# Kernel optimization log

Measured on AMD Instinct MI355X. Metric: run time of the kernel, lower is better.

Reference implementation:

```python
import jax, jax.numpy as jnp
import numpy as np

B, N, D = 32, 2048, 1024


def setup_inputs() -> dict:
    key = jax.random.key(0)
    k1, k2, k3, k4, k5, k6 = jax.random.split(key, 6)
    encoded = jax.random.normal(k1, (B, N, D), dtype=jnp.float32)
    decoder_state = jax.random.normal(k2, (B, D), dtype=jnp.float32)
    mask = jax.random.randint(k3, (B, N), 0, 2, dtype=jnp.int32)
    scale = 1.0 / np.sqrt(D)
    W1 = jax.random.normal(k4, (D, D), dtype=jnp.float32) * scale  # applied as x @ W1
    W2 = jax.random.normal(k5, (D, D), dtype=jnp.float32) * scale
    vt = jax.random.normal(k6, (D,), dtype=jnp.float32) * scale
    return {"encoded": encoded, "decoder_state": decoder_state, "mask": mask,
            "W1": W1, "W2": W2, "vt": vt}


def reference(encoded, decoder_state, mask, W1, W2, vt):
    temperature = 1.0
    # process_encoded: W1(encoded)  [B, N, D]
    enc = jnp.einsum('bnd,de->bne', encoded, W1)
    # W2(decoder_state)  [B, D] -> broadcast-add over N
    dec = decoder_state @ W2
    # vt(tanh(.)).squeeze(2)  -> logits [B, N]
    u = jnp.einsum('bnd,d->bn', jnp.tanh(enc + dec[:, None, :]), vt)
    # masked log-softmax with temperature over dim=1
    logits = u / temperature + jnp.log(mask.astype(u.dtype) + 1e-45)
    return jax.nn.log_softmax(logits, axis=1)
```

## Files before the change

### kernel.cpp

```cpp
#include <hip/hip_runtime.h>

typedef _Float16 half8 __attribute__((ext_vector_type(8)));
typedef __fp16   pk2   __attribute__((ext_vector_type(2)));
typedef float    f32x4 __attribute__((ext_vector_type(4)));

#define GLOBAL_AS __attribute__((address_space(1)))
#define LDS_AS    __attribute__((address_space(3)))

static constexpr int Bb = 32;
static constexpr int Nn = 2048;
static constexpr int Dd = 1024;
static constexpr int M  = Bb * Nn;

__global__ void prep_w1(const float* __restrict__ W1, _Float16* __restrict__ W1TT) {
    int g = blockIdx.x * 256 + threadIdx.x;
    int tile = g >> 9;
    int u = g & 511;
    int et = tile >> 5, kt = tile & 31;
    int q = u >> 7, e = u & 127;
    int d0 = kt * 32 + q * 8;
    int col = et * 128 + e;
    half8 h;
#pragma unroll
    for (int j = 0; j < 8; ++j)
        h[j] = (_Float16)W1[(size_t)(d0 + j) * Dd + col];
    *(half8*)(W1TT + (size_t)g * 8) = h;
}

__global__ void dec_kernel(const float* __restrict__ ds, const float* __restrict__ W2,
                           float* __restrict__ dec) {
    __shared__ float part[4][64];
    int b = blockIdx.x, ech = blockIdx.y;
    int tid = threadIdx.x;
    int e = ech * 64 + (tid & 63);
    int dc = tid >> 6;
    float acc = 0.f;
#pragma unroll 4
    for (int d = dc * 256; d < dc * 256 + 256; ++d)
        acc += ds[b * Dd + d] * W2[(size_t)d * Dd + e];
    part[dc][tid & 63] = acc;
    __syncthreads();
    if (tid < 64)
        dec[b * Dd + e] = part[0][tid] + part[1][tid] + part[2][tid] + part[3][tid];
}

__global__ __launch_bounds__(256) void gemm_fused(
    const float* __restrict__ A,
    const _Float16* __restrict__ W1TT,
    const float* __restrict__ dec,
    const float* __restrict__ vt,
    float* __restrict__ u_part)
{
    __shared__ _Float16 As2[4 * 128 * 8];
    __shared__ _Float16 Bs2[512 * 8];
    __shared__ float usum[2][128];

    const int et = blockIdx.x;
    const int mtile = blockIdx.y;
    const int tid = threadIdx.x;
    const int lane = tid & 63, wid = tid >> 6;
    const int wm = wid & 1, we = wid >> 1;
    const int q = lane >> 4, l15 = lane & 15;

    f32x4 acc[4][4] = {};

    const int arow = tid >> 1, khalf = tid & 1;
    const float* aptr = A + (size_t)(mtile * 128 + arow) * Dd + khalf * 16;
    const int q0 = khalf * 2;
    const _Float16* bbase = W1TT + (size_t)et * 32 * 512 * 8
                            + ((size_t)(wid * 2) * 64 + lane) * 8;
    _Float16* bdst0 = &Bs2[(wid * 2 + 0) * 64 * 8];
    _Float16* bdst1 = &Bs2[(wid * 2 + 1) * 64 * 8];

#pragma unroll 1
    for (int kt = 0; kt < 32; ++kt) {
        const _Float16* bk = bbase + (size_t)kt * 512 * 8;
        __builtin_amdgcn_global_load_lds((const GLOBAL_AS void*)bk,
                                         (LDS_AS void*)bdst0, 16, 0, 0);
        __builtin_amdgcn_global_load_lds((const GLOBAL_AS void*)(bk + 64 * 8),
                                         (LDS_AS void*)bdst1, 16, 0, 0);
        const float4* ap = (const float4*)(aptr + kt * 32);
        float4 f0 = ap[0], f1 = ap[1], f2 = ap[2], f3 = ap[3];
        half8 h0, h1;
        {
            pk2 t;
            t = __builtin_amdgcn_cvt_pkrtz(f0.x, f0.y); h0[0] = t[0]; h0[1] = t[1];
            t = __builtin_amdgcn_cvt_pkrtz(f0.z, f0.w); h0[2] = t[0]; h0[3] = t[1];
            t = __builtin_amdgcn_cvt_pkrtz(f1.x, f1.y); h0[4] = t[0]; h0[5] = t[1];
            t = __builtin_amdgcn_cvt_pkrtz(f1.z, f1.w); h0[6] = t[0]; h0[7] = t[1];
            t = __builtin_amdgcn_cvt_pkrtz(f2.x, f2.y); h1[0] = t[0]; h1[1] = t[1];
            t = __builtin_amdgcn_cvt_pkrtz(f2.z, f2.w); h1[2] = t[0]; h1[3] = t[1];
            t = __builtin_amdgcn_cvt_pkrtz(f3.x, f3.y); h1[4] = t[0]; h1[5] = t[1];
            t = __builtin_amdgcn_cvt_pkrtz(f3.z, f3.w); h1[6] = t[0]; h1[7] = t[1];
        }
        *(half8*)&As2[((q0 + 0) * 128 + arow) * 8] = h0;
        *(half8*)&As2[((q0 + 1) * 128 + arow) * 8] = h1;
        __syncthreads();

        half8 af[4], bf[4];
#pragma unroll
        for (int mt = 0; mt < 4; ++mt)
            af[mt] = *(const half8*)&As2[(q * 128 + wm * 64 + mt * 16 + l15) * 8];
#pragma unroll
        for (int nt = 0; nt < 4; ++nt)
            bf[nt] = *(const half8*)&Bs2[(q * 128 + we * 64 + nt * 16 + l15) * 8];
#pragma unroll
        for (int mt = 0; mt < 4; ++mt)
#pragma unroll
            for (int nt = 0; nt < 4; ++nt)
                acc[mt][nt] = __builtin_amdgcn_mfma_f32_16x16x32_f16(
                    af[mt], bf[nt], acc[mt][nt], 0, 0, 0);
        __syncthreads();
    }

    const int b = mtile >> 4;
    float vtv[4], dcv[4];
#pragma unroll
    for (int nt = 0; nt < 4; ++nt) {
        int e = et * 128 + we * 64 + nt * 16 + l15;
        vtv[nt] = vt[e];
        dcv[nt] = dec[b * Dd + e];
    }
#pragma unroll
    for (int mt = 0; mt < 4; ++mt) {
#pragma unroll
        for (int r = 0; r < 4; ++r) {
            float s = 0.f;
#pragma unroll
            for (int nt = 0; nt < 4; ++nt) {
                float x = acc[mt][nt][r] + dcv[nt];
                float ex = __expf(2.f * x);
                float th = 1.f - 2.f * __builtin_amdgcn_rcpf(ex + 1.f);
                s += th * vtv[nt];
            }
#pragma unroll
            for (int off = 1; off < 16; off <<= 1) s += __shfl_xor(s, off, 16);
            if (l15 == 0) usum[we][wm * 64 + mt * 16 + q * 4 + r] = s;
        }
    }
    __syncthreads();
    if (tid < 128)
        u_part[(size_t)et * M + (size_t)mtile * 128 + tid] = usum[0][tid] + usum[1][tid];
}

__global__ void softmax_k(const float* __restrict__ up, const int* __restrict__ mask,
                          float* __restrict__ out) {
    __shared__ float red[8];
    int b = blockIdx.x, tid = threadIdx.x;
    float l[8];
#pragma unroll
    for (int i = 0; i < 8; ++i) {
        int n = i * 256 + tid;
        float s = up[(size_t)b * Nn + n];
#pragma unroll
        for (int et = 1; et < 8; ++et) s += up[(size_t)et * M + (size_t)b * Nn + n];
        l[i] = s + (mask[b * Nn + n] ? 0.f : -103.278931f);
    }
    float m = l[0];
#pragma unroll
    for (int i = 1; i < 8; ++i) m = fmaxf(m, l[i]);
#pragma unroll
    for (int o = 32; o >= 1; o >>= 1) m = fmaxf(m, __shfl_xor(m, o, 64));
    if ((tid & 63) == 0) red[tid >> 6] = m;
    __syncthreads();
    m = fmaxf(fmaxf(red[0], red[1]), fmaxf(red[2], red[3]));
    float s = 0.f;
#pragma unroll
    for (int i = 0; i < 8; ++i) s += expf(l[i] - m);
#pragma unroll
    for (int o = 32; o >= 1; o >>= 1) s += __shfl_xor(s, o, 64);
    if ((tid & 63) == 0) red[4 + (tid >> 6)] = s;
    __syncthreads();
    float lse = m + logf(red[4] + red[5] + red[6] + red[7]);
#pragma unroll
    for (int i = 0; i < 8; ++i)
        out[(size_t)b * Nn + i * 256 + tid] = l[i] - lse;
}

extern "C" void kernel_launch(void* const* d_in, const int* in_sizes, int n_in,
                              void* d_out, int out_size, void* d_ws, size_t ws_size,
                              hipStream_t stream) {
    const float* encoded = (const float*)d_in[0];
    const float* dstate  = (const float*)d_in[1];
    const int*   mask    = (const int*)d_in[2];
    const float* W1      = (const float*)d_in[3];
    const float* W2      = (const float*)d_in[4];
    const float* vt      = (const float*)d_in[5];
    float* out = (float*)d_out;

    char* ws = (char*)d_ws;
    float*    u_part = (float*)ws;
    float*    dec    = (float*)(ws + (size_t)8 * M * 4);
    _Float16* W1TT   = (_Float16*)(ws + (size_t)8 * M * 4 + (size_t)Bb * Dd * 4);

    prep_w1<<<512, 256, 0, stream>>>(W1, W1TT);
    dec_kernel<<<dim3(32, 16), 256, 0, stream>>>(dstate, W2, dec);
    gemm_fused<<<dim3(8, 512), 256, 0, stream>>>(encoded, W1TT, dec, vt, u_part);
    softmax_k<<<32, 256, 0, stream>>>(u_part, mask, out);
}
```

Measured before the change: 622.2 us.

## Pre-convert encoded to fp16 tiled layout and stream both GEMM operands via LDS DMA

Adds a prep kernel that converts the encoded activations to fp16 in a tile-packed layout, so the fused GEMM can load A with global_load_lds directly into shared memory, the same way it loads B. This takes the per-iteration fp32 loads and conversions out of the GEMM's inner loop and halves the bytes each of the 8 column-tile blocks rereads. In exchange it adds a full extra pass that reads 256MB of fp32 and writes 128MB of fp16, and it needs a large workspace, with the old kernel kept as a fallback when the workspace is too small.

```diff
diff --git a/kernel.cpp b/kernel.cpp
--- a/kernel.cpp
+++ b/kernel.cpp
@@ -25,6 +25,24 @@
     for (int j = 0; j < 8; ++j)
         h[j] = (_Float16)W1[(size_t)(d0 + j) * Dd + col];
     *(half8*)(W1TT + (size_t)g * 8) = h;
+}
+
+__global__ void prep_enc(const float* __restrict__ A, _Float16* __restrict__ A_p) {
+    int g = blockIdx.x * 256 + threadIdx.x;
+    int tile = g >> 9;
+    int v = g & 511;
+    int row = v >> 2, kc = v & 3;
+    const float* src = A + ((size_t)(tile >> 5) * 128 + row) * Dd
+                         + (tile & 31) * 32 + kc * 8;
+    f32x4 f0 = *(const f32x4*)src;
+    f32x4 f1 = *(const f32x4*)(src + 4);
+    half8 h;
+    pk2 t;
+    t = __builtin_amdgcn_cvt_pkrtz(f0.x, f0.y); h[0] = t[0]; h[1] = t[1];
+    t = __builtin_amdgcn_cvt_pkrtz(f0.z, f0.w); h[2] = t[0]; h[3] = t[1];
+    t = __builtin_amdgcn_cvt_pkrtz(f1.x, f1.y); h[4] = t[0]; h[5] = t[1];
+    t = __builtin_amdgcn_cvt_pkrtz(f1.z, f1.w); h[6] = t[0]; h[7] = t[1];
+    *(half8*)(A_p + (size_t)g * 8) = h;
 }
 
 __global__ void dec_kernel(const float* __restrict__ ds, const float* __restrict__ W2,
@@ -44,15 +62,15 @@
         dec[b * Dd + e] = part[0][tid] + part[1][tid] + part[2][tid] + part[3][tid];
 }
 
-__global__ __launch_bounds__(256) void gemm_fused(
-    const float* __restrict__ A,
+__global__ __launch_bounds__(256) void gemm_fused_h(
+    const _Float16* __restrict__ A_p,
     const _Float16* __restrict__ W1TT,
     const float* __restrict__ dec,
     const float* __restrict__ vt,
     float* __restrict__ u_part)
 {
-    __shared__ _Float16 As2[4 * 128 * 8];
-    __shared__ _Float16 Bs2[512 * 8];
+    __shared__ _Float16 As[4096];
+    __shared__ _Float16 Bs[4096];
     __shared__ float usum[2][128];
 
     const int et = blockIdx.x;
@@ -64,17 +82,102 @@
 
     f32x4 acc[4][4] = {};
 
+    const _Float16* abase = A_p + (size_t)mtile * 32 * 4096
+                            + ((size_t)(wid * 2) * 64 + lane) * 8;
+    const _Float16* bbase = W1TT + (size_t)et * 32 * 4096
+                            + ((size_t)(wid * 2) * 64 + lane) * 8;
+    _Float16* adst0 = &As[(wid * 2 + 0) * 64 * 8];
+    _Float16* adst1 = &As[(wid * 2 + 1) * 64 * 8];
+    _Float16* bdst0 = &Bs[(wid * 2 + 0) * 64 * 8];
+    _Float16* bdst1 = &Bs[(wid * 2 + 1) * 64 * 8];
+
+#pragma unroll 1
+    for (int kt = 0; kt < 32; ++kt) {
+        const _Float16* ak = abase + (size_t)kt * 4096;
+        const _Float16* bk = bbase + (size_t)kt * 4096;
+        __builtin_amdgcn_global_load_lds((const GLOBAL_AS void*)ak,
+                                         (LDS_AS void*)adst0, 16, 0, 0);
+        __builtin_amdgcn_global_load_lds((const GLOBAL_AS void*)(ak + 64 * 8),
+                                         (LDS_AS void*)adst1, 16, 0, 0);
+        __builtin_amdgcn_global_load_lds((const GLOBAL_AS void*)bk,
+                                         (LDS_AS void*)bdst0, 16, 0, 0);
+        __builtin_amdgcn_global_load_lds((const GLOBAL_AS void*)(bk + 64 * 8),
+                                         (LDS_AS void*)bdst1, 16, 0, 0);
+        __syncthreads();
+
+        half8 af[4], bf[4];
+#pragma unroll
+        for (int mt = 0; mt < 4; ++mt)
+            af[mt] = *(const half8*)&As[(wm * 64 + mt * 16 + l15) * 32 + q * 8];
+#pragma unroll
+        for (int nt = 0; nt < 4; ++nt)
+            bf[nt] = *(const half8*)&Bs[(q * 128 + we * 64 + nt * 16 + l15) * 8];
+#pragma unroll
+        for (int mt = 0; mt < 4; ++mt)
+#pragma unroll
+            for (int nt = 0; nt < 4; ++nt)
+                acc[mt][nt] = __builtin_amdgcn_mfma_f32_16x16x32_f16(
+                    af[mt], bf[nt], acc[mt][nt], 0, 0, 0);
+        __syncthreads();
+    }
+
+    const int b = mtile >> 4;
+    float vtv[4], dcv[4];
+#pragma unroll
+    for (int nt = 0; nt < 4; ++nt) {
+        int e = et * 128 + we * 64 + nt * 16 + l15;
+        vtv[nt] = vt[e];
+        dcv[nt] = dec[b * Dd + e];
+    }
+#pragma unroll
+    for (int mt = 0; mt < 4; ++mt) {
+#pragma unroll
+        for (int r = 0; r < 4; ++r) {
+            float s = 0.f;
+#pragma unroll
+            for (int nt = 0; nt < 4; ++nt) {
+                float x = acc[mt][nt][r] + dcv[nt];
+                float ex = __expf(2.f * x);
+                float th = 1.f - 2.f * __builtin_amdgcn_rcpf(ex + 1.f);
+                s += th * vtv[nt];
+            }
+#pragma unroll
+            for (int off = 1; off < 16; off <<= 1) s += __shfl_xor(s, off, 16);
+            if (l15 == 0) usum[we][wm * 64 + mt * 16 + q * 4 + r] = s;
+        }
+    }
+    __syncthreads();
+    if (tid < 128)
+        u_part[(size_t)et * M + (size_t)mtile * 128 + tid] = usum[0][tid] + usum[1][tid];
+}
+
+__global__ __launch_bounds__(256) void gemm_fused_f32(
+    const float* __restrict__ A, const _Float16* __restrict__ W1TT,
+    const float* __restrict__ dec, const float* __restrict__ vt,
+    float* __restrict__ u_part)
+{
+    __shared__ _Float16 As2[4 * 128 * 8];
+    __shared__ _Float16 Bs2[512 * 8];
+    __shared__ float usum[2][128];
+
+    const int et = blockIdx.x, mtile = blockIdx.y;
+    const int tid = threadIdx.x;
+    const int lane = tid & 63, wid = tid >> 6;
+    const int wm = wid & 1, we = wid >> 1;
+    const int q = lane >> 4, l15 = lane & 15;
+    f32x4 acc[4][4] = {};
+
     const int arow = tid >> 1, khalf = tid & 1;
     const float* aptr = A + (size_t)(mtile * 128 + arow) * Dd + khalf * 16;
     const int q0 = khalf * 2;
-    const _Float16* bbase = W1TT + (size_t)et * 32 * 512 * 8
+    const _Float16* bbase = W1TT + (size_t)et * 32 * 4096
                             + ((size_t)(wid * 2) * 64 + lane) * 8;
     _Float16* bdst0 = &Bs2[(wid * 2 + 0) * 64 * 8];
     _Float16* bdst1 = &Bs2[(wid * 2 + 1) * 64 * 8];
 
 #pragma unroll 1
     for (int kt = 0; kt < 32; ++kt) {
-        const _Float16* bk = bbase + (size_t)kt * 512 * 8;
+        const _Float16* bk = bbase + (size_t)kt * 4096;
         __builtin_amdgcn_global_load_lds((const GLOBAL_AS void*)bk,
                                          (LDS_AS void*)bdst0, 16, 0, 0);
         __builtin_amdgcn_global_load_lds((const GLOBAL_AS void*)(bk + 64 * 8),
@@ -192,9 +295,18 @@
     float*    u_part = (float*)ws;
     float*    dec    = (float*)(ws + (size_t)8 * M * 4);
     _Float16* W1TT   = (_Float16*)(ws + (size_t)8 * M * 4 + (size_t)Bb * Dd * 4);
+    _Float16* A_p    = (_Float16*)(ws + (size_t)8 * M * 4 + (size_t)Bb * Dd * 4
+                                   + (size_t)Dd * Dd * 2);
+    const size_t needed = (size_t)8 * M * 4 + (size_t)Bb * Dd * 4
+                        + (size_t)Dd * Dd * 2 + (size_t)M * Dd * 2;
 
     prep_w1<<<512, 256, 0, stream>>>(W1, W1TT);
     dec_kernel<<<dim3(32, 16), 256, 0, stream>>>(dstate, W2, dec);
-    gemm_fused<<<dim3(8, 512), 256, 0, stream>>>(encoded, W1TT, dec, vt, u_part);
+    if (ws_size >= needed) {
+        prep_enc<<<32768, 256, 0, stream>>>(encoded, A_p);
+        gemm_fused_h<<<dim3(8, 512), 256, 0, stream>>>(A_p, W1TT, dec, vt, u_part);
+    } else {
+        gemm_fused_f32<<<dim3(8, 512), 256, 0, stream>>>(encoded, W1TT, dec, vt, u_part);
+    }
     softmax_k<<<32, 256, 0, stream>>>(u_part, mask, out);
 }
```

New measurement: 619.3 us. No clear change (-0.5%).
